# Optimization experiments

Hardware: AMD Instinct MI355X
Metric: run time of the kernel (lower is better)

Reference implementation:

```python
import jax, jax.numpy as jnp
import numpy as np

BLOCK = 32  # GGUF Q8_0 block size


def setup_inputs() -> dict:
    key = jax.random.key(0)
    k1, k2, k3, k4 = jax.random.split(key, 4)
    O, I = 11008, 4096
    x = jax.random.normal(k1, (32, I), dtype=jnp.float32)
    qweight = jax.random.randint(k2, (O, I), 0, 255, dtype=jnp.int32)
    scales = jax.random.uniform(k3, (O, I // BLOCK), dtype=jnp.float32) * 0.01
    bias = jax.random.normal(k4, (O,), dtype=jnp.float32)
    return {"x": x, "qweight": qweight, "scales": scales, "bias": bias}


def dequantize(qweight, scales):
    # Q8_0-style: signed int8 quants, one fp scale per block of 32 along in-dim.
    O, I = qweight.shape
    q = (qweight.astype(scales.dtype) - 127.0).reshape(O, I // BLOCK, BLOCK)
    w = q * scales[:, :, None]  # [O, nb, BLOCK]
    return w.reshape(O, I)


def reference(x, qweight, scales, bias):
    # On-the-fly dequant fused with F.linear: y = x @ W^T + b
    w = dequantize(qweight, scales)           # [O, I]
    return jnp.einsum('bi,oi->bo', x, w) + bias
```

## Files before the change

### kernel.cpp

```cpp
#include <hip/hip_runtime.h>
#include <hip/hip_bf16.h>


#define O_DIM 11008
#define I_DIM 4096
#define NB    128
#define B_DIM 32
#define NT    64
#define KT    1024
#define KS    128

typedef __attribute__((ext_vector_type(8))) short bf16x8;
typedef __attribute__((ext_vector_type(4))) float f32x4;

static __device__ __forceinline__ unsigned short f2bf(float f) {
    __hip_bfloat16 h = __float2bfloat16(f);
    return __builtin_bit_cast(unsigned short, h);
}

__global__ __launch_bounds__(256) void init_kernel(const float* __restrict__ x,
                                                   const float* __restrict__ bias,
                                                   float* __restrict__ out,
                                                   unsigned short* __restrict__ xbf) {
    const int gid = blockIdx.x * 256 + threadIdx.x;
    const int b = gid / O_DIM;
    const int o = gid - b * O_DIM;
    out[gid] = bias[o];
    if (gid < (B_DIM * I_DIM) / 4) {
        const float4 v = reinterpret_cast<const float4*>(x)[gid];
        ushort4 u;
        u.x = f2bf(v.x); u.y = f2bf(v.y); u.z = f2bf(v.z); u.w = f2bf(v.w);
        reinterpret_cast<ushort4*>(xbf)[gid] = u;
    }
}

__global__ __launch_bounds__(256) void gemm_mfma_kernel(const unsigned short* __restrict__ xbf,
                                                        const int*   __restrict__ qw,
                                                        const float* __restrict__ scales,
                                                        float*       __restrict__ out) {
    __shared__ unsigned short w_s[NT * KS];
    __shared__ unsigned short x_s[B_DIM * KS];

    const int t      = threadIdx.x;
    const int wav    = t >> 6;
    const int lan    = t & 63;
    const int o_base = blockIdx.x * NT;
    const int k_base = blockIdx.y * KT;

    const int so = t >> 2;
    const int sk = (t & 3) * 32;

    const int n0   = wav * 16;
    const int lrow = lan & 15;
    const int lq   = lan >> 4;
    const int swz  = (lrow & 7) << 4;

    f32x4 acc0 = {0.f, 0.f, 0.f, 0.f};
    f32x4 acc1 = {0.f, 0.f, 0.f, 0.f};

    for (int ks = 0; ks < KT; ks += KS) {
        const int kg = k_base + ks;

#pragma unroll
        for (int j = 0; j < 2; ++j) {
            const int idx = t + j * 256;
            const int m   = idx >> 4;
            const int kc  = (idx & 15) * 8;
            const bf16x8 v = *reinterpret_cast<const bf16x8*>(&xbf[m * I_DIM + kg + kc]);
            const int addr = ((m * KS + kc) * 2) ^ ((m & 7) << 4);
            *reinterpret_cast<bf16x8*>(reinterpret_cast<char*>(x_s) + addr) = v;
        }

        {
            const int   o = o_base + so;
            const float s = scales[o * NB + ((kg + sk) >> 5)];
            const float c = -127.0f * s;
            const int4* src = reinterpret_cast<const int4*>(&qw[o * I_DIM + kg + sk]);
#pragma unroll
            for (int ch = 0; ch < 4; ++ch) {
                const int4 qa = src[ch * 2 + 0];
                const int4 qb = src[ch * 2 + 1];
                bf16x8 v;
                v[0] = (short)f2bf(fmaf((float)qa.x, s, c));
                v[1] = (short)f2bf(fmaf((float)qa.y, s, c));
                v[2] = (short)f2bf(fmaf((float)qa.z, s, c));
                v[3] = (short)f2bf(fmaf((float)qa.w, s, c));
                v[4] = (short)f2bf(fmaf((float)qb.x, s, c));
                v[5] = (short)f2bf(fmaf((float)qb.y, s, c));
                v[6] = (short)f2bf(fmaf((float)qb.z, s, c));
                v[7] = (short)f2bf(fmaf((float)qb.w, s, c));
                const int addr = ((so * KS + sk + ch * 8) * 2) ^ ((so & 7) << 4);
                *reinterpret_cast<bf16x8*>(reinterpret_cast<char*>(w_s) + addr) = v;
            }
        }

        __syncthreads();

#pragma unroll
        for (int k4 = 0; k4 < 4; ++k4) {
            const int kb = k4 * 32 + lq * 8;
            const int a0addr = ((lrow * KS + kb) * 2) ^ swz;
            const int a1addr = (((lrow + 16) * KS + kb) * 2) ^ swz;
            const int baddr  = (((n0 + lrow) * KS + kb) * 2) ^ swz;
            const bf16x8 a0 = *reinterpret_cast<const bf16x8*>(reinterpret_cast<const char*>(x_s) + a0addr);
            const bf16x8 a1 = *reinterpret_cast<const bf16x8*>(reinterpret_cast<const char*>(x_s) + a1addr);
            const bf16x8 bb = *reinterpret_cast<const bf16x8*>(reinterpret_cast<const char*>(w_s) + baddr);
            acc0 = __builtin_amdgcn_mfma_f32_16x16x32_bf16(a0, bb, acc0, 0, 0, 0);
            acc1 = __builtin_amdgcn_mfma_f32_16x16x32_bf16(a1, bb, acc1, 0, 0, 0);
        }

        __syncthreads();
    }

    const int oc = o_base + n0 + lrow;
#pragma unroll
    for (int r = 0; r < 4; ++r) {
        const int m = lq * 4 + r;
        atomicAdd(&out[m * O_DIM + oc],          acc0[r]);
        atomicAdd(&out[(m + 16) * O_DIM + oc],   acc1[r]);
    }
}

extern "C" void kernel_launch(void* const* d_in, const int* in_sizes, int n_in,
                              void* d_out, int out_size, void* d_ws, size_t ws_size,
                              hipStream_t stream) {
    const float* x      = (const float*)d_in[0];
    const int*   qw     = (const int*)d_in[1];
    const float* scales = (const float*)d_in[2];
    const float* bias   = (const float*)d_in[3];
    float*       out    = (float*)d_out;
    unsigned short* xbf = (unsigned short*)d_ws;

    hipLaunchKernelGGL(init_kernel, dim3((B_DIM * O_DIM) / 256), dim3(256), 0, stream,
                       x, bias, out, xbf);

    hipLaunchKernelGGL(gemm_mfma_kernel, dim3(O_DIM / NT, I_DIM / KT), dim3(256), 0, stream,
                       xbf, qw, scales, out);
}
```

Baseline: 50.26 us.

## Stream dequantized weights directly into MFMA registers without LDS staging

Replaces the shared-memory tiled GEMM with a register-direct kernel: each lane loads its own int32 quant fragment and bf16 activation fragment from global memory, dequantizes in registers and feeds MFMA, with a one-step software prefetch. It also preloads the per-row scales into registers and raises the K split from 4 to 8 to create more blocks. This removes LDS writes, reads and barriers, at the cost of less coalesced global loads (each lane reads 32 bytes of a row, strided by rows) and twice as many atomic adds to the output.

After: 59.07 us. +17.5%, slower.

```diff
diff --git a/kernel.cpp b/kernel.cpp
--- a/kernel.cpp
+++ b/kernel.cpp
@@ -2,20 +2,19 @@
 #include <hip/hip_bf16.h>
 
 
-#define O_DIM 11008
-#define I_DIM 4096
-#define NB    128
-#define B_DIM 32
-#define NT    64
-#define KT    1024
-#define KS    128
+#define O_DIM  11008
+#define I_DIM  4096
+#define NB     128
+#define B_DIM  32
+#define NSPLIT 8
+#define KT     (I_DIM / NSPLIT)
+#define NSTEP  (KT / 32)
 
 typedef __attribute__((ext_vector_type(8))) short bf16x8;
 typedef __attribute__((ext_vector_type(4))) float f32x4;
 
 static __device__ __forceinline__ unsigned short f2bf(float f) {
-    __hip_bfloat16 h = __float2bfloat16(f);
-    return __builtin_bit_cast(unsigned short, h);
+    return __builtin_bit_cast(unsigned short, __float2bfloat16(f));
 }
 
 __global__ __launch_bounds__(256) void init_kernel(const float* __restrict__ x,
@@ -34,90 +33,80 @@
     }
 }
 
-__global__ __launch_bounds__(256) void gemm_mfma_kernel(const unsigned short* __restrict__ xbf,
-                                                        const int*   __restrict__ qw,
-                                                        const float* __restrict__ scales,
-                                                        float*       __restrict__ out) {
-    __shared__ unsigned short w_s[NT * KS];
-    __shared__ unsigned short x_s[B_DIM * KS];
+static __device__ __forceinline__ bf16x8 dequant8(const int4 qa, const int4 qb,
+                                                  const float s) {
+    const float c = -127.0f * s;
+    bf16x8 v;
+    v[0] = (short)f2bf(fmaf((float)qa.x, s, c));
+    v[1] = (short)f2bf(fmaf((float)qa.y, s, c));
+    v[2] = (short)f2bf(fmaf((float)qa.z, s, c));
+    v[3] = (short)f2bf(fmaf((float)qa.w, s, c));
+    v[4] = (short)f2bf(fmaf((float)qb.x, s, c));
+    v[5] = (short)f2bf(fmaf((float)qb.y, s, c));
+    v[6] = (short)f2bf(fmaf((float)qb.z, s, c));
+    v[7] = (short)f2bf(fmaf((float)qb.w, s, c));
+    return v;
+}
 
-    const int t      = threadIdx.x;
-    const int wav    = t >> 6;
-    const int lan    = t & 63;
-    const int o_base = blockIdx.x * NT;
-    const int k_base = blockIdx.y * KT;
-
-    const int so = t >> 2;
-    const int sk = (t & 3) * 32;
-
-    const int n0   = wav * 16;
+__global__ __launch_bounds__(256) void gemm_stream_kernel(const unsigned short* __restrict__ xbf,
+                                                          const int*   __restrict__ qw,
+                                                          const float* __restrict__ scales,
+                                                          float*       __restrict__ out) {
+    const int t    = threadIdx.x;
+    const int wav  = t >> 6;
+    const int lan  = t & 63;
     const int lrow = lan & 15;
     const int lq   = lan >> 4;
-    const int swz  = (lrow & 7) << 4;
+
+    const int o_base = blockIdx.x * 64 + wav * 16;
+    const int k_base = blockIdx.y * KT;
+    const int o_row  = o_base + lrow;
+
+    const int*            __restrict__ wq = qw  + o_row * I_DIM + k_base + lq * 8;
+    const unsigned short* __restrict__ xa = xbf + lrow * I_DIM + k_base + lq * 8;
+
+    float sc[NSTEP];
+    {
+        const float4* sp = reinterpret_cast<const float4*>(&scales[o_row * NB + (k_base >> 5)]);
+#pragma unroll
+        for (int j = 0; j < 4; ++j) {
+            const float4 v = sp[j];
+            sc[4 * j + 0] = v.x; sc[4 * j + 1] = v.y;
+            sc[4 * j + 2] = v.z; sc[4 * j + 3] = v.w;
+        }
+    }
 
     f32x4 acc0 = {0.f, 0.f, 0.f, 0.f};
     f32x4 acc1 = {0.f, 0.f, 0.f, 0.f};
 
-    for (int ks = 0; ks < KT; ks += KS) {
-        const int kg = k_base + ks;
+    int4   qa = *reinterpret_cast<const int4*>(wq);
+    int4   qb = *reinterpret_cast<const int4*>(wq + 4);
+    bf16x8 a0 = *reinterpret_cast<const bf16x8*>(xa);
+    bf16x8 a1 = *reinterpret_cast<const bf16x8*>(xa + 16 * I_DIM);
 
 #pragma unroll
-        for (int j = 0; j < 2; ++j) {
-            const int idx = t + j * 256;
-            const int m   = idx >> 4;
-            const int kc  = (idx & 15) * 8;
-            const bf16x8 v = *reinterpret_cast<const bf16x8*>(&xbf[m * I_DIM + kg + kc]);
-            const int addr = ((m * KS + kc) * 2) ^ ((m & 7) << 4);
-            *reinterpret_cast<bf16x8*>(reinterpret_cast<char*>(x_s) + addr) = v;
+    for (int s = 0; s < NSTEP; ++s) {
+        int4 nqa = {}, nqb = {};
+        bf16x8 na0 = {}, na1 = {};
+        if (s + 1 < NSTEP) {
+            const int*            w2 = wq + (s + 1) * 32;
+            const unsigned short* x2 = xa + (s + 1) * 32;
+            nqa = *reinterpret_cast<const int4*>(w2);
+            nqb = *reinterpret_cast<const int4*>(w2 + 4);
+            na0 = *reinterpret_cast<const bf16x8*>(x2);
+            na1 = *reinterpret_cast<const bf16x8*>(x2 + 16 * I_DIM);
         }
-
-        {
-            const int   o = o_base + so;
-            const float s = scales[o * NB + ((kg + sk) >> 5)];
-            const float c = -127.0f * s;
-            const int4* src = reinterpret_cast<const int4*>(&qw[o * I_DIM + kg + sk]);
-#pragma unroll
-            for (int ch = 0; ch < 4; ++ch) {
-                const int4 qa = src[ch * 2 + 0];
-                const int4 qb = src[ch * 2 + 1];
-                bf16x8 v;
-                v[0] = (short)f2bf(fmaf((float)qa.x, s, c));
-                v[1] = (short)f2bf(fmaf((float)qa.y, s, c));
-                v[2] = (short)f2bf(fmaf((float)qa.z, s, c));
-                v[3] = (short)f2bf(fmaf((float)qa.w, s, c));
-                v[4] = (short)f2bf(fmaf((float)qb.x, s, c));
-                v[5] = (short)f2bf(fmaf((float)qb.y, s, c));
-                v[6] = (short)f2bf(fmaf((float)qb.z, s, c));
-                v[7] = (short)f2bf(fmaf((float)qb.w, s, c));
-                const int addr = ((so * KS + sk + ch * 8) * 2) ^ ((so & 7) << 4);
-                *reinterpret_cast<bf16x8*>(reinterpret_cast<char*>(w_s) + addr) = v;
-            }
-        }
-
-        __syncthreads();
-
-#pragma unroll
-        for (int k4 = 0; k4 < 4; ++k4) {
-            const int kb = k4 * 32 + lq * 8;
-            const int a0addr = ((lrow * KS + kb) * 2) ^ swz;
-            const int a1addr = (((lrow + 16) * KS + kb) * 2) ^ swz;
-            const int baddr  = (((n0 + lrow) * KS + kb) * 2) ^ swz;
-            const bf16x8 a0 = *reinterpret_cast<const bf16x8*>(reinterpret_cast<const char*>(x_s) + a0addr);
-            const bf16x8 a1 = *reinterpret_cast<const bf16x8*>(reinterpret_cast<const char*>(x_s) + a1addr);
-            const bf16x8 bb = *reinterpret_cast<const bf16x8*>(reinterpret_cast<const char*>(w_s) + baddr);
-            acc0 = __builtin_amdgcn_mfma_f32_16x16x32_bf16(a0, bb, acc0, 0, 0, 0);
-            acc1 = __builtin_amdgcn_mfma_f32_16x16x32_bf16(a1, bb, acc1, 0, 0, 0);
-        }
-
-        __syncthreads();
+        const bf16x8 bfrag = dequant8(qa, qb, sc[s]);
+        acc0 = __builtin_amdgcn_mfma_f32_16x16x32_bf16(a0, bfrag, acc0, 0, 0, 0);
+        acc1 = __builtin_amdgcn_mfma_f32_16x16x32_bf16(a1, bfrag, acc1, 0, 0, 0);
+        qa = nqa; qb = nqb; a0 = na0; a1 = na1;
     }
 
-    const int oc = o_base + n0 + lrow;
 #pragma unroll
     for (int r = 0; r < 4; ++r) {
         const int m = lq * 4 + r;
-        atomicAdd(&out[m * O_DIM + oc],          acc0[r]);
-        atomicAdd(&out[(m + 16) * O_DIM + oc],   acc1[r]);
+        atomicAdd(&out[m * O_DIM + o_row],        acc0[r]);
+        atomicAdd(&out[(m + 16) * O_DIM + o_row], acc1[r]);
     }
 }
 
@@ -134,6 +123,6 @@
     hipLaunchKernelGGL(init_kernel, dim3((B_DIM * O_DIM) / 256), dim3(256), 0, stream,
                        x, bias, out, xbf);
 
-    hipLaunchKernelGGL(gemm_mfma_kernel, dim3(O_DIM / NT, I_DIM / KT), dim3(256), 0, stream,
+    hipLaunchKernelGGL(gemm_stream_kernel, dim3(O_DIM / 64, NSPLIT), dim3(256), 0, stream,
                        xbf, qw, scales, out);
 }
```
